# Kernel tuning notes

Measured on AMD Instinct MI355X. Metric: run time of the kernel, lower is better.

Reference implementation:

```python
import jax, jax.numpy as jnp
import numpy as np

B, H_, W_, C, HEADS, WS, SR = 4, 56, 56, 256, 8, 3, 4
HD = C // HEADS
N = H_ * W_
LL = WS * WS
PH, PW = H_ // SR, W_ // SR
PL = PH * PW
K_TAB = 2048


def _unfold3(x, H, W):
    # x: (B, C, H, W) -> (B, C, 9, H*W); matches torch nn.Unfold(kernel_size=3, padding=1)
    xp = jnp.pad(x, ((0, 0), (0, 0), (1, 1), (1, 1)))
    pats = jnp.stack([xp[:, :, i:i + H, j:j + W] for i in range(3) for j in range(3)], axis=2)
    return pats.reshape(x.shape[0], x.shape[1], 9, H * W)


def _l2n(x):
    # torch F.normalize(dim=-1) with eps=1e-12
    return x / jnp.maximum(jnp.linalg.norm(x, axis=-1, keepdims=True), 1e-12)


def setup_inputs() -> dict:
    key = jax.random.key(0)
    ks = jax.random.split(key, 24)
    x = jax.random.normal(ks[0], (B, N, C), jnp.float32)
    # padding mask from unfold of ones image (True where window element falls outside)
    ones = np.zeros((H_ + 2, W_ + 2), np.float32)
    ones[1:-1, 1:-1] = 1.0
    pats = np.stack([ones[i:i + H_, j:j + W_] for i in range(3) for j in range(3)], 0).reshape(9, N)
    padding_mask = jnp.asarray((pats == 0).T)  # (N, 9) bool
    local_valid = LL - padding_mask.sum(-1)
    seq_length_scale = jnp.log(local_valid.astype(jnp.float32) + PL)[:, None]  # (N,1)
    relative_pos_index = jax.random.randint(ks[1], (N * PL,), 0, K_TAB)
    relative_coords_table = jax.random.uniform(ks[2], (K_TAB, 2), jnp.float32, -1.0, 1.0)
    w = lambda k, shape: jax.random.normal(k, shape, jnp.float32) * 0.02
    inp = dict(
        x=x, H=H_, W=W_,
        relative_pos_index=relative_pos_index,
        relative_coords_table=relative_coords_table,
        seq_length_scale=seq_length_scale,
        padding_mask=padding_mask,
        q_w=w(ks[3], (C, C)), q_b=jnp.zeros((C,), jnp.float32),
        kv_w=w(ks[4], (2 * C, C)), kv_b=jnp.zeros((2 * C,), jnp.float32),
        sr_w=w(ks[5], (C, C)), sr_b=jnp.zeros((C,), jnp.float32),
        norm_g=jnp.ones((C,), jnp.float32), norm_b=jnp.zeros((C,), jnp.float32),
        cpb1_w=w(ks[6], (512, 2)), cpb1_b=jnp.zeros((512,), jnp.float32),
        cpb2_w=w(ks[7], (HEADS, 512)), cpb2_b=jnp.zeros((HEADS,), jnp.float32),
        temperature=jnp.log(jnp.exp(jnp.ones((HEADS, 1, 1), jnp.float32) / 0.24) - 1.0),
        query_embedding=w(ks[8], (HEADS, 1, HD)),
        rel_pos_bias_local=jax.random.normal(ks[9], (HEADS, LL), jnp.float32) * 0.0004,
        learnable_tokens=w(ks[10], (HEADS, HD, LL)),
        learnable_bias=jnp.zeros((HEADS, 1, LL), jnp.float32),
        proj_w=w(ks[11], (C, C)), proj_b=jnp.zeros((C,), jnp.float32),
    )
    return inp


def reference(x, H, W, relative_pos_index, relative_coords_table, seq_length_scale,
              padding_mask, q_w, q_b, kv_w, kv_b, sr_w, sr_b, norm_g, norm_b,
              cpb1_w, cpb1_b, cpb2_w, cpb2_b, temperature, query_embedding,
              rel_pos_bias_local, learnable_tokens, learnable_bias, proj_w, proj_b):
    Bsz, n, Cd = x.shape
    h, hd, ll = HEADS, HD, LL
    pH, pW = H // SR, W // SR
    pL = pH * pW
    # ----- queries -----
    q = (x @ q_w.T + q_b).reshape(Bsz, n, h, hd).transpose(0, 2, 1, 3)  # (B,h,N,d)
    q_norm = _l2n(q)
    q_scaled = (q_norm + query_embedding) * jax.nn.softplus(temperature) * seq_length_scale
    # ----- local branch: unfolded window KV -----
    kv = x @ kv_w.T + kv_b  # (B,N,2C)
    k_loc, v_loc = jnp.split(kv, 2, axis=-1)
    k_loc = _l2n(k_loc.reshape(Bsz, n, h, hd)).reshape(Bsz, n, Cd)
    kv_img = jnp.concatenate([k_loc, v_loc], -1).transpose(0, 2, 1).reshape(Bsz, 2 * Cd, H, W)
    pats = _unfold3(kv_img, H, W).reshape(Bsz, 2 * h, hd, ll, n).transpose(0, 1, 4, 2, 3)  # (B,2h,N,d,ll)
    k_local, v_local = jnp.split(pats, 2, axis=1)
    attn_local = jnp.einsum('bhnd,bhndl->bhnl', q_scaled, k_local) + rel_pos_bias_local[:, None, :]
    attn_local = jnp.where(padding_mask, -jnp.inf, attn_local)
    # ----- global branch: 1x1 conv -> GELU -> avg pool -> LN -> KV -----
    x_img = x.transpose(0, 2, 1).reshape(Bsz, Cd, H, W)
    x_sr = jax.nn.gelu(jnp.einsum('oc,bchw->bohw', sr_w, x_img) + sr_b[None, :, None, None], approximate=False)
    x_pool = x_sr.reshape(Bsz, Cd, pH, SR, pW, SR).mean(axis=(3, 5)).reshape(Bsz, Cd, pL).transpose(0, 2, 1)
    mu = x_pool.mean(-1, keepdims=True)
    var = x_pool.var(-1, keepdims=True)
    x_pool = (x_pool - mu) / jnp.sqrt(var + 1e-5) * norm_g + norm_b
    kvp = (x_pool @ kv_w.T + kv_b).reshape(Bsz, pL, 2 * h, hd).transpose(0, 2, 1, 3)
    k_pool, v_pool = jnp.split(kvp, 2, axis=1)  # each (B,h,pL,d)
    # CPB-MLP relative position bias (interpolate is identity since test==trained resolution)
    tab = jax.nn.relu(relative_coords_table @ cpb1_w.T + cpb1_b) @ cpb2_w.T + cpb2_b  # (K,h)
    pool_bias = tab.T[:, relative_pos_index].reshape(h, n, pL)
    attn_pool = jnp.einsum('bhnd,bhmd->bhnm', q_scaled, _l2n(k_pool)) + pool_bias
    # ----- joint softmax over [local | pool] -----
    attn = jax.nn.softmax(jnp.concatenate([attn_local, attn_pool], axis=-1), axis=-1)
    a_loc, a_pool = attn[..., :ll], attn[..., ll:]
    w_loc = jnp.einsum('bhnd,hdl->bhnl', q_norm, learnable_tokens) + learnable_bias + a_loc
    x_local = jnp.einsum('bhnl,bhndl->bhnd', w_loc, v_local)
    x_glob = jnp.einsum('bhnm,bhmd->bhnd', a_pool, v_pool)
    out = (x_local + x_glob).transpose(0, 2, 1, 3).reshape(Bsz, n, Cd)
    return out @ proj_w.T + proj_b
```

## Files before the change

kernel.cpp:

```cpp
#include <hip/hip_runtime.h>
#include <hip/hip_bf16.h>
#include <math.h>

#define Bn   4
#define Hh   56
#define Wn   56
#define Cn   256
#define NHn  8
#define HDn  32
#define Nn   3136
#define LLn  9
#define PLn  196
#define PWn  14
#define KTABn 2048
#define Mrows 12544
#define MP   224

#define XCNT   3211264
#define QWOFF  XCNT
#define KVWOFF (QWOFF + 65536)
#define SRWOFF (KVWOFF + 131072)
#define PWOFF  (SRWOFF + 65536)
#define TOTCVT (PWOFF + 65536)

typedef __attribute__((ext_vector_type(8))) short short8v;
typedef __attribute__((ext_vector_type(4))) float float4v;

__device__ __forceinline__ unsigned short f2b(float f) {
  __hip_bfloat16 h = __float2bfloat16(f);
  return *(unsigned short*)&h;
}
__device__ __forceinline__ float b2f(unsigned short u) {
  union { unsigned int i; float f; } x; x.i = ((unsigned int)u) << 16; return x.f;
}
__device__ __forceinline__ void u4_to8f(uint4 u, float* o) {
  o[0]=b2f((unsigned short)(u.x&0xffff)); o[1]=b2f((unsigned short)(u.x>>16));
  o[2]=b2f((unsigned short)(u.y&0xffff)); o[3]=b2f((unsigned short)(u.y>>16));
  o[4]=b2f((unsigned short)(u.z&0xffff)); o[5]=b2f((unsigned short)(u.z>>16));
  o[6]=b2f((unsigned short)(u.w&0xffff)); o[7]=b2f((unsigned short)(u.w>>16));
}

__launch_bounds__(256)
__global__ void cvt5(const float* __restrict__ x, const float* __restrict__ qw,
                     const float* __restrict__ kvw, const float* __restrict__ srw,
                     const float* __restrict__ pw, unsigned short* __restrict__ dst)
{
  const int i = (blockIdx.x * 256 + threadIdx.x) * 4;
  const float* src; int off;
  if      (i < XCNT)   { src = x;   off = 0; }
  else if (i < KVWOFF) { src = qw;  off = QWOFF; }
  else if (i < SRWOFF) { src = kvw; off = KVWOFF; }
  else if (i < PWOFF)  { src = srw; off = SRWOFF; }
  else                 { src = pw;  off = PWOFF; }
  const float4 v = *(const float4*)(src + (i - off));
  ushort4 o2;
  o2.x = f2b(v.x); o2.y = f2b(v.y); o2.z = f2b(v.z); o2.w = f2b(v.w);
  *(ushort4*)(dst + i) = o2;
}

template <int MODE>
__launch_bounds__(512)
__global__ void mgemm(const unsigned short* __restrict__ A,
                      const unsigned short* __restrict__ Wb,
                      const float* __restrict__ b0, const float* __restrict__ b1,
                      const float* __restrict__ b2, void* __restrict__ Cv, int Nc,
                      const float* __restrict__ sls, const float* __restrict__ qe,
                      const float* __restrict__ temp, float* __restrict__ Mq)
{
  __shared__ __align__(16) unsigned char smem[34816];
  unsigned short* As = (unsigned short*)smem;
  unsigned short* Bs = (unsigned short*)(smem + 16384);
  const int t = threadIdx.x;
  const int w = t >> 6, lane = t & 63;
  const int q = lane >> 4, ln = lane & 15;
  const int n0 = blockIdx.x * 128, m0 = blockIdx.y * 128;
  const int wm = (w >> 1) * 32, wn = (w & 1) * 64;

  float4v acc[2][4];
  #pragma unroll
  for (int mt = 0; mt < 2; ++mt)
    #pragma unroll
    for (int nt = 0; nt < 4; ++nt)
      acc[mt][nt] = (float4v){0.f, 0.f, 0.f, 0.f};

  for (int k0 = 0; k0 < 256; k0 += 64) {
    #pragma unroll
    for (int j = 0; j < 2; ++j) {
      const int u = t + 512 * j;
      const int r = u >> 3, cg = u & 7;
      const int cs = cg ^ (r & 7);
      const uint4 av = *(const uint4*)(A  + (size_t)(m0 + r) * 256 + k0 + cg * 8);
      *(uint4*)(As + r * 64 + cs * 8) = av;
      const uint4 bv = *(const uint4*)(Wb + (size_t)(n0 + r) * 256 + k0 + cg * 8);
      *(uint4*)(Bs + r * 64 + cs * 8) = bv;
    }
    __syncthreads();
    #pragma unroll
    for (int kk = 0; kk < 2; ++kk) {
      short8v af[2], bfr[4];
      const int cg = kk * 4 + q;
      #pragma unroll
      for (int mt = 0; mt < 2; ++mt) {
        const int r = wm + mt * 16 + ln;
        af[mt] = *(const short8v*)(As + r * 64 + (cg ^ (r & 7)) * 8);
      }
      #pragma unroll
      for (int nt = 0; nt < 4; ++nt) {
        const int r = wn + nt * 16 + ln;
        bfr[nt] = *(const short8v*)(Bs + r * 64 + (cg ^ (r & 7)) * 8);
      }
      #pragma unroll
      for (int mt = 0; mt < 2; ++mt)
        #pragma unroll
        for (int nt = 0; nt < 4; ++nt)
          acc[mt][nt] = __builtin_amdgcn_mfma_f32_16x16x32_bf16(af[mt], bfr[nt], acc[mt][nt], 0, 0, 0);
    }
    __syncthreads();
  }

  if constexpr (MODE == 0) {
    float* C = (float*)Cv;
    float* tileF = (float*)smem;
    float bia[4];
    #pragma unroll
    for (int nt = 0; nt < 4; ++nt) bia[nt] = b0[n0 + wn + nt * 16 + ln];
    #pragma unroll
    for (int half = 0; half < 2; ++half) {
      if ((w >> 2) == half) {
        #pragma unroll
        for (int mt = 0; mt < 2; ++mt)
          #pragma unroll
          for (int r = 0; r < 4; ++r)
            #pragma unroll
            for (int nt = 0; nt < 4; ++nt)
              tileF[(wm - half*64 + mt*16 + q*4 + r) * 132 + wn + nt*16 + ln] = acc[mt][nt][r] + bia[nt];
      }
      __syncthreads();
      #pragma unroll
      for (int j = 0; j < 4; ++j) {
        const int i = j * 512 + t;
        const int row = i >> 5, ch = i & 31;
        float4 v = *(const float4*)(tileF + row * 132 + ch * 4);
        *(float4*)(C + (size_t)(m0 + half * 64 + row) * Nc + n0 + ch * 4) = v;
      }
      __syncthreads();
    }
  } else {
    unsigned short* Cb = (unsigned short*)Cv;
    unsigned short* tileC = (unsigned short*)smem;
    const int seg = n0 >> 8;
    const int h0 = (n0 + wn) >> 5, h1 = h0 + 1;
    float spt0 = 0.f, spt1 = 0.f;
    if (seg == 0) { spt0 = log1pf(__expf(temp[h0])); spt1 = log1pf(__expf(temp[h1])); }
    float bia[4], qev[4];
    #pragma unroll
    for (int nt = 0; nt < 4; ++nt) {
      const int col = n0 + wn + nt * 16 + ln;
      bia[nt] = (seg == 0) ? b0[col] : (seg == 3 ? b2[col - 768] : b1[col - 256]);
      if (seg == 0) qev[nt] = qe[col];
    }
    #pragma unroll
    for (int mt = 0; mt < 2; ++mt) {
      #pragma unroll
      for (int r = 0; r < 4; ++r) {
        const int row = m0 + wm + mt * 16 + q * 4 + r;
        const int lrow = wm + mt * 16 + q * 4 + r;
        float vals[4];
        #pragma unroll
        for (int nt = 0; nt < 4; ++nt) vals[nt] = acc[mt][nt][r] + bia[nt];
        if (seg == 0) {
          float ss0 = vals[0]*vals[0] + vals[1]*vals[1];
          float ss1 = vals[2]*vals[2] + vals[3]*vals[3];
          #pragma unroll
          for (int mk = 1; mk <= 8; mk <<= 1) { ss0 += __shfl_xor(ss0, mk); ss1 += __shfl_xor(ss1, mk); }
          const float i0 = 1.f / fmaxf(sqrtf(ss0), 1e-12f);
          const float i1 = 1.f / fmaxf(sqrtf(ss1), 1e-12f);
          const int nidx = row % Nn, bb = row / Nn;
          const float sl = sls[nidx];
          float qsv[4];
          #pragma unroll
          for (int nt = 0; nt < 4; ++nt) {
            const float inv = (nt < 2) ? i0 : i1;
            const float sp  = (nt < 2) ? spt0 : spt1;
            qsv[nt] = (vals[nt] * inv + qev[nt]) * sp * sl;
          }
          float t0 = qsv[0]*qsv[0] + qsv[1]*qsv[1];
          float t1 = qsv[2]*qsv[2] + qsv[3]*qsv[3];
          #pragma unroll
          for (int mk = 1; mk <= 8; mk <<= 1) { t0 += __shfl_xor(t0, mk); t1 += __shfl_xor(t1, mk); }
          if (ln == 0) {
            Mq[((size_t)(bb * NHn + h0)) * Nn + nidx] = sqrtf(t0);
            Mq[((size_t)(bb * NHn + h1)) * Nn + nidx] = sqrtf(t1);
          }
          #pragma unroll
          for (int nt = 0; nt < 4; ++nt)
            tileC[lrow * 136 + wn + nt*16 + ln] = f2b(qsv[nt]);
        } else if (seg == 1) {
          float ss0 = vals[0]*vals[0] + vals[1]*vals[1];
          float ss1 = vals[2]*vals[2] + vals[3]*vals[3];
          #pragma unroll
          for (int mk = 1; mk <= 8; mk <<= 1) { ss0 += __shfl_xor(ss0, mk); ss1 += __shfl_xor(ss1, mk); }
          const float i0 = 1.f / fmaxf(sqrtf(ss0), 1e-12f);
          const float i1 = 1.f / fmaxf(sqrtf(ss1), 1e-12f);
          #pragma unroll
          for (int nt = 0; nt < 4; ++nt)
            tileC[lrow * 136 + wn + nt*16 + ln] = f2b(vals[nt] * ((nt < 2) ? i0 : i1));
        } else if (seg == 2) {
          #pragma unroll
          for (int nt = 0; nt < 4; ++nt)
            tileC[lrow * 136 + wn + nt*16 + ln] = f2b(vals[nt]);
        } else {
          #pragma unroll
          for (int nt = 0; nt < 4; ++nt) {
            const float v = vals[nt];
            tileC[lrow * 136 + wn + nt*16 + ln] =
              f2b(0.5f * v * (1.0f + erff(v * 0.70710678118654752f)));
          }
        }
      }
    }
    __syncthreads();
    #pragma unroll
    for (int j = 0; j < 4; ++j) {
      const int i = j * 512 + t;
      const int row = i >> 4, ch = i & 15;
      uint4 v = *(const uint4*)(tileC + row * 136 + ch * 8);
      *(uint4*)(Cb + (size_t)(m0 + row) * 1024 + n0 + ch * 8) = v;
    }
  }
}

__launch_bounds__(256)
__global__ void gemm_k(const float* __restrict__ A, const float* __restrict__ W,
                       const float* __restrict__ bias, float* __restrict__ Co,
                       int Mr, int Nc, int K)
{
  __shared__ __align__(16) float As[16][64];
  __shared__ __align__(16) float Ws[16][64];
  const int t  = threadIdx.x;
  const int m0 = blockIdx.y * 64, n0 = blockIdx.x * 64;
  const int lm = t >> 2, lk = (t & 3) << 2;
  const int tx = t & 15, ty = t >> 4;
  float acc[4][4] = {};
  int arow = m0 + lm; if (arow >= Mr) arow = Mr - 1;
  const int wrow = n0 + lm;
  for (int k0 = 0; k0 < K; k0 += 16) {
    float4 av = *(const float4*)(A + (size_t)arow * K + k0 + lk);
    As[lk+0][lm] = av.x; As[lk+1][lm] = av.y; As[lk+2][lm] = av.z; As[lk+3][lm] = av.w;
    float4 wv = *(const float4*)(W + (size_t)wrow * K + k0 + lk);
    Ws[lk+0][lm] = wv.x; Ws[lk+1][lm] = wv.y; Ws[lk+2][lm] = wv.z; Ws[lk+3][lm] = wv.w;
    __syncthreads();
    #pragma unroll
    for (int k = 0; k < 16; ++k) {
      float4 a = *(const float4*)&As[k][ty << 2];
      float4 w = *(const float4*)&Ws[k][tx << 2];
      acc[0][0] += a.x*w.x; acc[0][1] += a.x*w.y; acc[0][2] += a.x*w.z; acc[0][3] += a.x*w.w;
      acc[1][0] += a.y*w.x; acc[1][1] += a.y*w.y; acc[1][2] += a.y*w.z; acc[1][3] += a.y*w.w;
      acc[2][0] += a.z*w.x; acc[2][1] += a.z*w.y; acc[2][2] += a.z*w.z; acc[2][3] += a.z*w.w;
      acc[3][0] += a.w*w.x; acc[3][1] += a.w*w.y; acc[3][2] += a.w*w.z; acc[3][3] += a.w*w.w;
    }
    __syncthreads();
  }
  #pragma unroll
  for (int i = 0; i < 4; ++i) {
    const int row = m0 + (ty << 2) + i;
    if (row >= Mr) continue;
    #pragma unroll
    for (int j = 0; j < 4; ++j) {
      const int col = n0 + (tx << 2) + j;
      Co[(size_t)row * Nc + col] = acc[i][j] + bias[col];
    }
  }
}

__launch_bounds__(256)
__global__ void pool_ln_k(const unsigned short* __restrict__ fused, float* __restrict__ pln,
                          const float* __restrict__ g, const float* __restrict__ bb)
{
  const int blk = blockIdx.x;
  const int b = blk / PLn, pc = blk % PLn;
  const int pi = pc / PWn, pj = pc % PWn;
  const int c = threadIdx.x;
  float s = 0.f;
  #pragma unroll
  for (int r = 0; r < 4; ++r)
    #pragma unroll
    for (int cc = 0; cc < 4; ++cc) {
      const int n = (pi*4 + r) * Wn + pj*4 + cc;
      s += b2f(fused[((size_t)b * Nn + n) * 1024 + 768 + c]);
    }
  s *= (1.f/16.f);
  float sum = s, sq = s*s;
  #pragma unroll
  for (int m = 32; m >= 1; m >>= 1) { sum += __shfl_xor(sum, m); sq += __shfl_xor(sq, m); }
  __shared__ float sm[8];
  const int lane = c & 63, wid = c >> 6;
  if (lane == 0) { sm[wid] = sum; sm[4+wid] = sq; }
  __syncthreads();
  const float tot  = sm[0]+sm[1]+sm[2]+sm[3];
  const float totq = sm[4]+sm[5]+sm[6]+sm[7];
  const float mu  = tot * (1.f/256.f);
  const float var = totq * (1.f/256.f) - mu*mu;
  pln[(size_t)blk * Cn + c] = (s - mu) / sqrtf(var + 1e-5f) * g[c] + bb[c];
}

__launch_bounds__(256)
__global__ void pool_pack(const float* __restrict__ kvp, unsigned short* __restrict__ kbf,
                          unsigned short* __restrict__ vbf)
{
  const int bh = blockIdx.x;
  const int b = bh >> 3, h = bh & 7;
  const int t = threadIdx.x, mg = t >> 5, d = t & 31;
  for (int mi = 0; mi < MP/8; ++mi) {
    const int m = mi * 8 + mg;
    float kv2 = 0.f, vv = 0.f;
    if (m < PLn) {
      kv2 = kvp[((size_t)(b * PLn + m)) * 512 + h * HDn + d];
      vv  = kvp[((size_t)(b * PLn + m)) * 512 + 256 + h * HDn + d];
    }
    float ssn = kv2 * kv2;
    #pragma unroll
    for (int mm = 16; mm >= 1; mm >>= 1) ssn += __shfl_xor(ssn, mm);
    const float kn = (m < PLn) ? kv2 / fmaxf(sqrtf(ssn), 1e-12f) : 0.f;
    kbf[((size_t)bh * MP + m) * HDn + d] = f2b(kn);
    vbf[((size_t)bh * 33 + d) * MP + m] = f2b(vv);
  }
  for (int i = t; i < MP; i += 256)
    vbf[((size_t)bh * 33 + 32) * MP + i] = f2b(1.0f);
}

__launch_bounds__(64)
__global__ void cpb_k(const float* __restrict__ rct, const float* __restrict__ w1,
                      const float* __restrict__ b1, const float* __restrict__ w2,
                      const float* __restrict__ b2, float* __restrict__ tab)
{
  const int r = blockIdx.x, t = threadIdx.x;
  const float c0 = rct[r*2], c1 = rct[r*2+1];
  float part[8] = {};
  #pragma unroll
  for (int jj = 0; jj < 8; ++jj) {
    const int j = t * 8 + jj;
    float hv = fmaxf(c0 * w1[j*2] + c1 * w1[j*2+1] + b1[j], 0.f);
    #pragma unroll
    for (int h = 0; h < 8; ++h) part[h] += hv * w2[h*512 + j];
  }
  #pragma unroll
  for (int h = 0; h < 8; ++h)
    for (int mm = 32; mm >= 1; mm >>= 1) part[h] += __shfl_xor(part[h], mm);
  if (t < 8) tab[r*8 + t] = part[t] + b2[t];
}

__launch_bounds__(256)
__global__ void redmax_k(const float* __restrict__ tab, const float* __restrict__ rpb,
                         float* __restrict__ scal)
{
  float mx = -1e30f;
  for (int i = threadIdx.x; i < KTABn*NHn; i += 256) mx = fmaxf(mx, tab[i]);
  if (threadIdx.x < NHn*LLn) mx = fmaxf(mx, rpb[threadIdx.x]);
  #pragma unroll
  for (int m = 32; m >= 1; m >>= 1) mx = fmaxf(mx, __shfl_xor(mx, m));
  __shared__ float sm[4];
  if ((threadIdx.x & 63) == 0) sm[threadIdx.x >> 6] = mx;
  __syncthreads();
  if (threadIdx.x == 0) scal[0] = fmaxf(fmaxf(sm[0], sm[1]), fmaxf(sm[2], sm[3]));
}

__launch_bounds__(256)
__global__ void bias_g2(const int* __restrict__ rpi, const float* __restrict__ tab,
                        unsigned short* __restrict__ bias2)
{
  const int tid = blockIdx.x * 256 + threadIdx.x;
  const int n = tid / MP, m = tid - n * MP;
  if (m < PLn) {
    const int idx = rpi[(size_t)n * PLn + m];
    #pragma unroll
    for (int h = 0; h < NHn; ++h)
      bias2[((size_t)h * Nn + n) * MP + m] = f2b(tab[(size_t)idx * NHn + h]);
  } else {
    #pragma unroll
    for (int h = 0; h < NHn; ++h)
      bias2[((size_t)h * Nn + n) * MP + m] = 0xFF80;
  }
}

__launch_bounds__(256)
__global__ void attn_pool(const unsigned short* __restrict__ fused,
                          const unsigned short* __restrict__ kbf,
                          const unsigned short* __restrict__ vbf,
                          const unsigned short* __restrict__ bias2,
                          const float* __restrict__ Mq, const float* __restrict__ scal,
                          float* __restrict__ opart)
{
  __shared__ __align__(16) unsigned short sh[32256];
  unsigned short* k_lds = sh;
  unsigned short* v_lds = sh + 7168;
  unsigned short* p_lds = sh + 17920;
  const int t = threadIdx.x;
  const int w = t >> 6, lane = t & 63;
  const int ln = lane & 15, quad = lane >> 4;
  const int tile = blockIdx.x, h = blockIdx.y, b = blockIdx.z;
  const int bh = b * NHn + h;

  {
    const uint4* gk = (const uint4*)(kbf + (size_t)bh * (MP * HDn));
    uint4* lk = (uint4*)k_lds;
    for (int i = t; i < 896; i += 256) lk[i] = gk[i];
    const uint4* gv = (const uint4*)(vbf + (size_t)bh * (33 * MP));
    uint4* lv = (uint4*)v_lds;
    for (int i = t; i < 924; i += 256) lv[i] = gv[i];
  }
  __syncthreads();

  const int nb = tile * 64 + w * 16;
  const short8v afrag = *(const short8v*)(fused +
      ((size_t)(b * Nn + nb + ln)) * 1024 + h * HDn + quad * 8);
  float M4[4];
  const float sc = scal[0];
  #pragma unroll
  for (int r = 0; r < 4; ++r) M4[r] = Mq[(size_t)bh * Nn + nb + quad * 4 + r] + sc;

  unsigned short* pst = p_lds + w * (16 * MP);
  #pragma unroll
  for (int mt = 0; mt < 14; ++mt) {
    short8v bfrag = *(const short8v*)(k_lds + (mt * 16 + ln) * HDn + quad * 8);
    float4v s = __builtin_amdgcn_mfma_f32_16x16x32_bf16(afrag, bfrag,
                                                        (float4v){0.f,0.f,0.f,0.f}, 0, 0, 0);
    #pragma unroll
    for (int r = 0; r < 4; ++r) {
      const int nr = nb + quad * 4 + r;
      const float bv = b2f(bias2[((size_t)h * Nn + nr) * MP + mt * 16 + ln]);
      const float p = __expf(s[r] + bv - M4[r]);
      pst[(quad * 4 + r) * MP + mt * 16 + ln] = f2b(p);
    }
  }

  float4v accO[3];
  accO[0] = (float4v){0.f,0.f,0.f,0.f};
  accO[1] = (float4v){0.f,0.f,0.f,0.f};
  accO[2] = (float4v){0.f,0.f,0.f,0.f};
  #pragma unroll
  for (int kc = 0; kc < 7; ++kc) {
    short8v pa = *(const short8v*)(pst + ln * MP + kc * 32 + quad * 8);
    #pragma unroll
    for (int nt = 0; nt < 3; ++nt) {
      short8v vb = *(const short8v*)(v_lds + (nt * 16 + ln) * MP + kc * 32 + quad * 8);
      accO[nt] = __builtin_amdgcn_mfma_f32_16x16x32_bf16(pa, vb, accO[nt], 0, 0, 0);
    }
  }
  #pragma unroll
  for (int r = 0; r < 4; ++r) {
    const size_t base = ((size_t)bh * Nn + nb + quad * 4 + r) * 33;
    opart[base + ln]      = accO[0][r];
    opart[base + 16 + ln] = accO[1][r];
    if (ln == 0) opart[base + 32] = accO[2][r];
  }
}

__launch_bounds__(256, 2)
__global__ void attn_loc(const unsigned short* __restrict__ fused,
                         const float* __restrict__ slsp, const float* __restrict__ temp,
                         const float* __restrict__ qe, const float* __restrict__ lt,
                         const float* __restrict__ lb, const float* __restrict__ rpb,
                         const float* __restrict__ scal, const float* __restrict__ Mq,
                         const float* __restrict__ opart, unsigned short* __restrict__ outp)
{
  __shared__ float red[4 * 64 * 33];
  __shared__ float lt_s[HDn * LLn];
  __shared__ float qe_s[HDn];
  __shared__ float lb_s[LLn], rpb_s[LLn];
  const int t = threadIdx.x;
  const int w = t >> 6, lane = t & 63;
  const int tile = blockIdx.x, h = blockIdx.y, b = blockIdx.z;
  const int n = tile * 64 + lane;
  const int bh = b * NHn + h;

  for (int i = t; i < HDn * LLn; i += 256) lt_s[i] = lt[h * HDn * LLn + i];
  if (t < HDn) qe_s[t] = qe[h * HDn + t];
  if (t < LLn) { lb_s[t] = lb[h * LLn + t]; rpb_s[t] = rpb[h * LLn + t]; }
  __syncthreads();

  const unsigned short* qp = fused + ((size_t)(b * Nn + n)) * 1024 + h * HDn;
  float qs[HDn];
  #pragma unroll
  for (int i = 0; i < 4; ++i) u4_to8f(((const uint4*)qp)[i], qs + i * 8);
  const float M = Mq[(size_t)bh * Nn + n] + scal[0];

  float acc[HDn], ext[HDn];
  #pragma unroll
  for (int d = 0; d < HDn; ++d) { acc[d] = 0.f; ext[d] = 0.f; }
  float l_run = 0.f;

  const float spt = log1pf(__expf(temp[h]));
  const float inv_qs = 1.f / (spt * slsp[n]);
  const int pi = n / Wn, pj = n % Wn;
  for (int lc = w; lc < LLn; lc += 4) {
    const int ii = pi + lc/3 - 1, jj = pj + (lc%3) - 1;
    if (ii < 0 || ii >= Hh || jj < 0 || jj >= Wn) continue;
    const int nb2 = ii * Wn + jj;
    float e = lb_s[lc];
    #pragma unroll
    for (int d = 0; d < HDn; ++d) e += (qs[d]*inv_qs - qe_s[d]) * lt_s[d*LLn + lc];
    const unsigned short* kr = fused + ((size_t)(b * Nn + nb2)) * 1024 + 256 + h * HDn;
    float kk[HDn];
    #pragma unroll
    for (int i = 0; i < 4; ++i) u4_to8f(((const uint4*)kr)[i], kk + i * 8);
    float p0=0,p1=0,p2=0,p3=0;
    #pragma unroll
    for (int dq = 0; dq < 8; ++dq) {
      const int d = dq*4;
      p0 += qs[d]*kk[d]; p1 += qs[d+1]*kk[d+1]; p2 += qs[d+2]*kk[d+2]; p3 += qs[d+3]*kk[d+3];
    }
    const float p = __expf(((p0+p1)+(p2+p3) + rpb_s[lc]) - M);
    l_run += p;
    float vv[HDn];
    #pragma unroll
    for (int i = 0; i < 4; ++i) u4_to8f(((const uint4*)(kr + 256))[i], vv + i * 8);
    #pragma unroll
    for (int d = 0; d < HDn; ++d) { acc[d] += p * vv[d]; ext[d] += e * vv[d]; }
  }

  float* myred = red + (w * 64 + lane) * 33;
  #pragma unroll
  for (int d = 0; d < HDn; ++d) myred[d] = acc[d];
  myred[32] = l_run;
  __syncthreads();
  const int n2 = t >> 2, dg = t & 3;
  float o[8], l_tot;
  {
    const float* r0 = red + n2 * 33, *r1 = r0 + 64*33, *r2 = r1 + 64*33, *r3 = r2 + 64*33;
    l_tot = r0[32] + r1[32] + r2[32] + r3[32];
    #pragma unroll
    for (int j = 0; j < 8; ++j)
      o[j] = r0[dg*8+j] + r1[dg*8+j] + r2[dg*8+j] + r3[dg*8+j];
  }
  __syncthreads();
  #pragma unroll
  for (int d = 0; d < HDn; ++d) myred[d] = ext[d];
  __syncthreads();
  float et[8];
  {
    const float* r0 = red + n2 * 33, *r1 = r0 + 64*33, *r2 = r1 + 64*33, *r3 = r2 + 64*33;
    #pragma unroll
    for (int j = 0; j < 8; ++j)
      et[j] = r0[dg*8+j] + r1[dg*8+j] + r2[dg*8+j] + r3[dg*8+j];
  }
  const size_t obase = ((size_t)bh * Nn + tile * 64 + n2) * 33;
  const float l_pool = opart[obase + 32];
  float op[8];
  #pragma unroll
  for (int j = 0; j < 8; ++j) op[j] = opart[obase + dg * 8 + j];
  const float invl = 1.f / (l_tot + l_pool);
  uint4 u;
  u.x = f2b((o[0]+op[0])*invl+et[0]) | ((unsigned int)f2b((o[1]+op[1])*invl+et[1]) << 16);
  u.y = f2b((o[2]+op[2])*invl+et[2]) | ((unsigned int)f2b((o[3]+op[3])*invl+et[3]) << 16);
  u.z = f2b((o[4]+op[4])*invl+et[4]) | ((unsigned int)f2b((o[5]+op[5])*invl+et[5]) << 16);
  u.w = f2b((o[6]+op[6])*invl+et[6]) | ((unsigned int)f2b((o[7]+op[7])*invl+et[7]) << 16);
  *(uint4*)(outp + ((size_t)b * Nn + tile*64 + n2) * Cn + h * HDn + dg * 8) = u;
}

extern "C" void kernel_launch(void* const* d_in, const int* in_sizes, int n_in,
                              void* d_out, int out_size, void* d_ws, size_t ws_size,
                              hipStream_t stream)
{
  const float* x    = (const float*)d_in[0];
  const int*   rpi  = (const int*)d_in[3];
  const float* rct  = (const float*)d_in[4];
  const float* sls  = (const float*)d_in[5];
  const float* q_w  = (const float*)d_in[7];
  const float* q_b  = (const float*)d_in[8];
  const float* kv_w = (const float*)d_in[9];
  const float* kv_b = (const float*)d_in[10];
  const float* sr_w = (const float*)d_in[11];
  const float* sr_b = (const float*)d_in[12];
  const float* ng   = (const float*)d_in[13];
  const float* nbta = (const float*)d_in[14];
  const float* c1w  = (const float*)d_in[15];
  const float* c1b  = (const float*)d_in[16];
  const float* c2w  = (const float*)d_in[17];
  const float* c2b  = (const float*)d_in[18];
  const float* temp = (const float*)d_in[19];
  const float* qe   = (const float*)d_in[20];
  const float* rpb  = (const float*)d_in[21];
  const float* lt   = (const float*)d_in[22];
  const float* lb   = (const float*)d_in[23];
  const float* pw   = (const float*)d_in[24];
  const float* pb   = (const float*)d_in[25];

  float* ws = (float*)d_ws;
  size_t o = 0;
  unsigned short* bf = (unsigned short*)(ws + o); o += TOTCVT / 2;
  unsigned short* fused = (unsigned short*)(ws + o); o += (size_t)Mrows * 512;
  float* Mq    = ws + o;  o += (size_t)Bn * NHn * Nn;
  float* pln   = ws + o;  o += (size_t)Bn * PLn * Cn;
  float* kvp   = ws + o;  o += (size_t)Bn * PLn * 2 * Cn;
  unsigned short* kbf = (unsigned short*)(ws + o); o += (size_t)Bn * NHn * MP * HDn / 2;
  unsigned short* vbf = (unsigned short*)(ws + o); o += (size_t)Bn * NHn * 33 * MP / 2;
  float* tab   = ws + o;  o += (size_t)KTABn * NHn;
  float* scal  = ws + o;  o += 8;
  unsigned short* bias2 = (unsigned short*)(ws + o); o += (size_t)NHn * Nn * MP / 2;
  float* opart = ws + o;  o += (size_t)Bn * NHn * Nn * 33;
  unsigned short* outp  = (unsigned short*)(ws + o); o += (size_t)Mrows * Cn / 2;

  const unsigned short* xbf   = bf;
  const unsigned short* qkvsw = bf + QWOFF;
  const unsigned short* pwbf  = bf + PWOFF;

  cvt5<<<TOTCVT/1024, 256, 0, stream>>>(x, q_w, kv_w, sr_w, pw, bf);
  mgemm<1><<<dim3(8, 98), 512, 0, stream>>>(xbf, qkvsw, q_b, kv_b, sr_b, fused, 1024,
                                            sls, qe, temp, Mq);
  pool_ln_k<<<Bn*PLn, 256, 0, stream>>>(fused, pln, ng, nbta);
  gemm_k<<<dim3(8, 13), 256, 0, stream>>>(pln, kv_w, kv_b, kvp, Bn*PLn, 512, 256);
  pool_pack<<<Bn*NHn, 256, 0, stream>>>(kvp, kbf, vbf);
  cpb_k<<<KTABn, 64, 0, stream>>>(rct, c1w, c1b, c2w, c2b, tab);
  redmax_k<<<1, 256, 0, stream>>>(tab, rpb, scal);
  bias_g2<<<(Nn*MP)/256, 256, 0, stream>>>(rpi, tab, bias2);
  attn_pool<<<dim3(49, NHn, Bn), 256, 0, stream>>>(fused, kbf, vbf, bias2, Mq, scal, opart);
  attn_loc<<<dim3(49, NHn, Bn), 256, 0, stream>>>(fused, sls, temp, qe, lt, lb,
                                                  rpb, scal, Mq, opart, outp);
  mgemm<0><<<dim3(2, 98), 512, 0, stream>>>(outp, pwbf, pb, pb, pb, (float*)d_out, 256,
                                            nullptr, nullptr, nullptr, nullptr);
}
```

Before: 270.9 us.

## Fuse pooled and local attention kernels, keep pool partials in LDS

Merges the pooled-attention MFMA kernel and the local-window attention kernel into one launch. The pooled partial outputs and row sums now stay in each wave's own LDS probability buffer instead of going through a global opart buffer, which removes a large intermediate write and read plus one launch. The local part is also reorganised: four lanes share one query, each covering 8 head dims and combining dot products with xor shuffles, replacing the old split over window positions and the block-wide LDS reduction with its extra barriers. In exchange the fused kernel carries more registers and its LDS footprint is shared across both phases, which may affect occupancy.

```diff
diff --git a/kernel.cpp b/kernel.cpp
--- a/kernel.cpp
+++ b/kernel.cpp
@@ -384,17 +384,25 @@
 }
 
 __launch_bounds__(256)
-__global__ void attn_pool(const unsigned short* __restrict__ fused,
-                          const unsigned short* __restrict__ kbf,
-                          const unsigned short* __restrict__ vbf,
-                          const unsigned short* __restrict__ bias2,
-                          const float* __restrict__ Mq, const float* __restrict__ scal,
-                          float* __restrict__ opart)
+__global__ void attn_f(const unsigned short* __restrict__ fused,
+                       const unsigned short* __restrict__ kbf,
+                       const unsigned short* __restrict__ vbf,
+                       const unsigned short* __restrict__ bias2,
+                       const float* __restrict__ Mq, const float* __restrict__ scal,
+                       const float* __restrict__ slsp, const float* __restrict__ temp,
+                       const float* __restrict__ qe, const float* __restrict__ lt,
+                       const float* __restrict__ lb, const float* __restrict__ rpb,
+                       unsigned short* __restrict__ outp)
 {
   __shared__ __align__(16) unsigned short sh[32256];
   unsigned short* k_lds = sh;
   unsigned short* v_lds = sh + 7168;
   unsigned short* p_lds = sh + 17920;
+  float* tabf = (float*)(v_lds + 33 * MP);
+  float* qe_s  = tabf;
+  float* lt_s  = tabf + 32;
+  float* lb_s  = tabf + 320;
+  float* rpb_s = tabf + 329;
   const int t = threadIdx.x;
   const int w = t >> 6, lane = t & 63;
   const int ln = lane & 15, quad = lane >> 4;
@@ -408,6 +416,9 @@
     const uint4* gv = (const uint4*)(vbf + (size_t)bh * (33 * MP));
     uint4* lv = (uint4*)v_lds;
     for (int i = t; i < 924; i += 256) lv[i] = gv[i];
+    if (t < 32) qe_s[t] = qe[h * HDn + t];
+    for (int i = t; i < HDn * LLn; i += 256) lt_s[i] = lt[h * HDn * LLn + i];
+    if (t < LLn) { lb_s[t] = lb[h * LLn + t]; rpb_s[t] = rpb[h * LLn + t]; }
   }
   __syncthreads();
 
@@ -447,115 +458,69 @@
       accO[nt] = __builtin_amdgcn_mfma_f32_16x16x32_bf16(pa, vb, accO[nt], 0, 0, 0);
     }
   }
+  float* pool_w = (float*)pst;
   #pragma unroll
   for (int r = 0; r < 4; ++r) {
-    const size_t base = ((size_t)bh * Nn + nb + quad * 4 + r) * 33;
-    opart[base + ln]      = accO[0][r];
-    opart[base + 16 + ln] = accO[1][r];
-    if (ln == 0) opart[base + 32] = accO[2][r];
-  }
-}
-
-__launch_bounds__(256, 2)
-__global__ void attn_loc(const unsigned short* __restrict__ fused,
-                         const float* __restrict__ slsp, const float* __restrict__ temp,
-                         const float* __restrict__ qe, const float* __restrict__ lt,
-                         const float* __restrict__ lb, const float* __restrict__ rpb,
-                         const float* __restrict__ scal, const float* __restrict__ Mq,
-                         const float* __restrict__ opart, unsigned short* __restrict__ outp)
-{
-  __shared__ float red[4 * 64 * 33];
-  __shared__ float lt_s[HDn * LLn];
-  __shared__ float qe_s[HDn];
-  __shared__ float lb_s[LLn], rpb_s[LLn];
-  const int t = threadIdx.x;
-  const int w = t >> 6, lane = t & 63;
-  const int tile = blockIdx.x, h = blockIdx.y, b = blockIdx.z;
-  const int n = tile * 64 + lane;
-  const int bh = b * NHn + h;
-
-  for (int i = t; i < HDn * LLn; i += 256) lt_s[i] = lt[h * HDn * LLn + i];
-  if (t < HDn) qe_s[t] = qe[h * HDn + t];
-  if (t < LLn) { lb_s[t] = lb[h * LLn + t]; rpb_s[t] = rpb[h * LLn + t]; }
-  __syncthreads();
-
-  const unsigned short* qp = fused + ((size_t)(b * Nn + n)) * 1024 + h * HDn;
-  float qs[HDn];
-  #pragma unroll
-  for (int i = 0; i < 4; ++i) u4_to8f(((const uint4*)qp)[i], qs + i * 8);
-  const float M = Mq[(size_t)bh * Nn + n] + scal[0];
-
-  float acc[HDn], ext[HDn];
-  #pragma unroll
-  for (int d = 0; d < HDn; ++d) { acc[d] = 0.f; ext[d] = 0.f; }
-  float l_run = 0.f;
-
+    const int row = quad * 4 + r;
+    pool_w[row * 33 + ln]      = accO[0][r];
+    pool_w[row * 33 + 16 + ln] = accO[1][r];
+    if (ln == 0) pool_w[row * 33 + 32] = accO[2][r];
+  }
+
+  const int nl = t >> 2, dg = t & 3;
+  const int n = tile * 64 + nl;
+  const unsigned short* qp = fused + ((size_t)(b * Nn + n)) * 1024 + h * HDn + dg * 8;
+  float qs8[8];
+  u4_to8f(*(const uint4*)qp, qs8);
+  const float M = Mq[(size_t)bh * Nn + n] + sc;
   const float spt = log1pf(__expf(temp[h]));
   const float inv_qs = 1.f / (spt * slsp[n]);
+
+  float acc8[8], ext8[8];
+  #pragma unroll
+  for (int j = 0; j < 8; ++j) { acc8[j] = 0.f; ext8[j] = 0.f; }
+  float l_run = 0.f;
   const int pi = n / Wn, pj = n % Wn;
-  for (int lc = w; lc < LLn; lc += 4) {
+  #pragma unroll
+  for (int lc = 0; lc < LLn; ++lc) {
     const int ii = pi + lc/3 - 1, jj = pj + (lc%3) - 1;
     if (ii < 0 || ii >= Hh || jj < 0 || jj >= Wn) continue;
     const int nb2 = ii * Wn + jj;
-    float e = lb_s[lc];
-    #pragma unroll
-    for (int d = 0; d < HDn; ++d) e += (qs[d]*inv_qs - qe_s[d]) * lt_s[d*LLn + lc];
-    const unsigned short* kr = fused + ((size_t)(b * Nn + nb2)) * 1024 + 256 + h * HDn;
-    float kk[HDn];
-    #pragma unroll
-    for (int i = 0; i < 4; ++i) u4_to8f(((const uint4*)kr)[i], kk + i * 8);
-    float p0=0,p1=0,p2=0,p3=0;
-    #pragma unroll
-    for (int dq = 0; dq < 8; ++dq) {
-      const int d = dq*4;
-      p0 += qs[d]*kk[d]; p1 += qs[d+1]*kk[d+1]; p2 += qs[d+2]*kk[d+2]; p3 += qs[d+3]*kk[d+3];
-    }
-    const float p = __expf(((p0+p1)+(p2+p3) + rpb_s[lc]) - M);
+    const unsigned short* kr = fused + ((size_t)(b * Nn + nb2)) * 1024 + 256 + h * HDn + dg * 8;
+    float kk8[8], vv8[8];
+    u4_to8f(*(const uint4*)kr, kk8);
+    u4_to8f(*(const uint4*)(kr + 256), vv8);
+    float pp = 0.f, ep = 0.f;
+    #pragma unroll
+    for (int j = 0; j < 8; ++j) {
+      pp += qs8[j] * kk8[j];
+      ep += (qs8[j] * inv_qs - qe_s[dg*8 + j]) * lt_s[(dg*8 + j) * LLn + lc];
+    }
+    pp += __shfl_xor(pp, 1); pp += __shfl_xor(pp, 2);
+    ep += __shfl_xor(ep, 1); ep += __shfl_xor(ep, 2);
+    const float e = ep + lb_s[lc];
+    const float p = __expf(pp + rpb_s[lc] - M);
     l_run += p;
-    float vv[HDn];
-    #pragma unroll
-    for (int i = 0; i < 4; ++i) u4_to8f(((const uint4*)(kr + 256))[i], vv + i * 8);
-    #pragma unroll
-    for (int d = 0; d < HDn; ++d) { acc[d] += p * vv[d]; ext[d] += e * vv[d]; }
-  }
-
-  float* myred = red + (w * 64 + lane) * 33;
-  #pragma unroll
-  for (int d = 0; d < HDn; ++d) myred[d] = acc[d];
-  myred[32] = l_run;
-  __syncthreads();
-  const int n2 = t >> 2, dg = t & 3;
-  float o[8], l_tot;
+    #pragma unroll
+    for (int j = 0; j < 8; ++j) { acc8[j] += p * vv8[j]; ext8[j] += e * vv8[j]; }
+  }
+
+  const float* pool_r = (float*)(p_lds + w * (16 * MP)) + (nl - w * 16) * 33;
+  const float l_pool = pool_r[32];
+  const float invl = 1.f / (l_run + l_pool);
+  uint4 u;
   {
-    const float* r0 = red + n2 * 33, *r1 = r0 + 64*33, *r2 = r1 + 64*33, *r3 = r2 + 64*33;
-    l_tot = r0[32] + r1[32] + r2[32] + r3[32];
-    #pragma unroll
-    for (int j = 0; j < 8; ++j)
-      o[j] = r0[dg*8+j] + r1[dg*8+j] + r2[dg*8+j] + r3[dg*8+j];
-  }
-  __syncthreads();
-  #pragma unroll
-  for (int d = 0; d < HDn; ++d) myred[d] = ext[d];
-  __syncthreads();
-  float et[8];
-  {
-    const float* r0 = red + n2 * 33, *r1 = r0 + 64*33, *r2 = r1 + 64*33, *r3 = r2 + 64*33;
-    #pragma unroll
-    for (int j = 0; j < 8; ++j)
-      et[j] = r0[dg*8+j] + r1[dg*8+j] + r2[dg*8+j] + r3[dg*8+j];
-  }
-  const size_t obase = ((size_t)bh * Nn + tile * 64 + n2) * 33;
-  const float l_pool = opart[obase + 32];
-  float op[8];
-  #pragma unroll
-  for (int j = 0; j < 8; ++j) op[j] = opart[obase + dg * 8 + j];
-  const float invl = 1.f / (l_tot + l_pool);
-  uint4 u;
-  u.x = f2b((o[0]+op[0])*invl+et[0]) | ((unsigned int)f2b((o[1]+op[1])*invl+et[1]) << 16);
-  u.y = f2b((o[2]+op[2])*invl+et[2]) | ((unsigned int)f2b((o[3]+op[3])*invl+et[3]) << 16);
-  u.z = f2b((o[4]+op[4])*invl+et[4]) | ((unsigned int)f2b((o[5]+op[5])*invl+et[5]) << 16);
-  u.w = f2b((o[6]+op[6])*invl+et[6]) | ((unsigned int)f2b((o[7]+op[7])*invl+et[7]) << 16);
-  *(uint4*)(outp + ((size_t)b * Nn + tile*64 + n2) * Cn + h * HDn + dg * 8) = u;
+    const float* op = pool_r + dg * 8;
+    float o0 = (acc8[0]+op[0])*invl + ext8[0], o1 = (acc8[1]+op[1])*invl + ext8[1];
+    float o2 = (acc8[2]+op[2])*invl + ext8[2], o3 = (acc8[3]+op[3])*invl + ext8[3];
+    float o4 = (acc8[4]+op[4])*invl + ext8[4], o5 = (acc8[5]+op[5])*invl + ext8[5];
+    float o6 = (acc8[6]+op[6])*invl + ext8[6], o7 = (acc8[7]+op[7])*invl + ext8[7];
+    u.x = f2b(o0) | ((unsigned int)f2b(o1) << 16);
+    u.y = f2b(o2) | ((unsigned int)f2b(o3) << 16);
+    u.z = f2b(o4) | ((unsigned int)f2b(o5) << 16);
+    u.w = f2b(o6) | ((unsigned int)f2b(o7) << 16);
+  }
+  *(uint4*)(outp + ((size_t)b * Nn + n) * Cn + h * HDn + dg * 8) = u;
 }
 
 extern "C" void kernel_launch(void* const* d_in, const int* in_sizes, int n_in,
@@ -598,7 +563,6 @@
   float* tab   = ws + o;  o += (size_t)KTABn * NHn;
   float* scal  = ws + o;  o += 8;
   unsigned short* bias2 = (unsigned short*)(ws + o); o += (size_t)NHn * Nn * MP / 2;
-  float* opart = ws + o;  o += (size_t)Bn * NHn * Nn * 33;
   unsigned short* outp  = (unsigned short*)(ws + o); o += (size_t)Mrows * Cn / 2;
 
   const unsigned short* xbf   = bf;
@@ -614,9 +578,8 @@
   cpb_k<<<KTABn, 64, 0, stream>>>(rct, c1w, c1b, c2w, c2b, tab);
   redmax_k<<<1, 256, 0, stream>>>(tab, rpb, scal);
   bias_g2<<<(Nn*MP)/256, 256, 0, stream>>>(rpi, tab, bias2);
-  attn_pool<<<dim3(49, NHn, Bn), 256, 0, stream>>>(fused, kbf, vbf, bias2, Mq, scal, opart);
-  attn_loc<<<dim3(49, NHn, Bn), 256, 0, stream>>>(fused, sls, temp, qe, lt, lb,
-                                                  rpb, scal, Mq, opart, outp);
+  attn_f<<<dim3(49, NHn, Bn), 256, 0, stream>>>(fused, kbf, vbf, bias2, Mq, scal,
+                                                sls, temp, qe, lt, lb, rpb, outp);
   mgemm<0><<<dim3(2, 98), 512, 0, stream>>>(outp, pwbf, pb, pb, pb, (float*)d_out, 256,
                                             nullptr, nullptr, nullptr, nullptr);
 }
```

New measurement: 261.5 us. 3.5% less time.
